# Optimization experiments

Hardware: AMD Instinct MI355X
Metric: run time of the kernel (lower is better)

## Reference

```python
import jax, jax.numpy as jnp
import numpy as np

B, S, D, H = 2, 2048, 1024, 16
DK = D // H

def setup_inputs() -> dict:
    key = jax.random.key(0)
    ks = jax.random.split(key, 11)
    scale = 1.0 / np.sqrt(D)
    inp = {
        'query': jax.random.normal(ks[0], (B, S, D), jnp.float32),
        'key':   jax.random.normal(ks[1], (B, S, D), jnp.float32),
        'value': jax.random.normal(ks[2], (B, S, D), jnp.float32),
        'wq': jax.random.normal(ks[3], (D, D), jnp.float32) * scale,
        'bq': jax.random.normal(ks[4], (D,), jnp.float32) * 0.01,
        'wk': jax.random.normal(ks[5], (D, D), jnp.float32) * scale,
        'bk': jax.random.normal(ks[6], (D,), jnp.float32) * 0.01,
        'wv': jax.random.normal(ks[7], (D, D), jnp.float32) * scale,
        'bv': jax.random.normal(ks[8], (D,), jnp.float32) * 0.01,
        'wo': jax.random.normal(ks[9], (D, D), jnp.float32) * scale,
        'bo': jax.random.normal(ks[10], (D,), jnp.float32) * 0.01,
    }
    return inp

def reference(query, key, value, wq, bq, wk, bk, wv, bv, wo, bo):
    nb = query.shape[0]
    # projections: torch nn.Linear computes x @ W^T + b; here weights stored as (in,out)
    def proj(x, w, b):
        return (x @ w + b).reshape(nb, -1, H, DK).transpose(0, 2, 1, 3)  # [B,H,S,dk]
    q = proj(query, wq, bq)
    k = proj(key, wk, bk)
    v = proj(value, wv, bv)
    scores = jnp.einsum('bhqd,bhkd->bhqk', q, k) / jnp.sqrt(jnp.float32(DK))
    p = jax.nn.softmax(scores, axis=-1)  # dropout p=0 (eval)
    x = jnp.einsum('bhqk,bhkd->bhqd', p, v)
    x = x.transpose(0, 2, 1, 3).reshape(nb, -1, H * DK)
    return x @ wo + bo
```

## Files before the change

### kernel.cpp

```cpp
#include <hip/hip_runtime.h>


typedef __attribute__((ext_vector_type(8))) __bf16 bf16x8;
typedef __attribute__((ext_vector_type(4))) __bf16 bf16x4;
typedef __attribute__((ext_vector_type(8))) float f32x8;
typedef __attribute__((ext_vector_type(4))) float f32x4;
typedef __attribute__((ext_vector_type(16))) float f32x16;
typedef unsigned uv2 __attribute__((ext_vector_type(2)));

#define MFMA16 __builtin_amdgcn_mfma_f32_16x16x32_bf16
#define MFMA32 __builtin_amdgcn_mfma_f32_32x32x16_bf16

union Bf8 { bf16x8 v; __bf16 e[8]; };

__device__ inline f32x4 zero4() { f32x4 z; z[0]=z[1]=z[2]=z[3]=0.f; return z; }
__device__ inline f32x16 zero16() {
    f32x16 z;
#pragma unroll
    for (int i = 0; i < 16; i++) z[i] = 0.f;
    return z;
}

__device__ inline float fast_exp2(float x) {
#if __has_builtin(__builtin_amdgcn_exp2f)
    return __builtin_amdgcn_exp2f(x);
#else
    return __expf(x * 0.6931471805599453f);
#endif
}

#if __has_builtin(__builtin_amdgcn_permlane32_swap)
#define HAVE_PLSWAP 1
#endif

__device__ inline void plswap32(unsigned &a, unsigned &b) {
#ifdef HAVE_PLSWAP
    uv2 r = __builtin_amdgcn_permlane32_swap(a, b, false, false);
    a = r[0]; b = r[1];
#else
    unsigned sa = __shfl_xor((int)a, 32), sb = __shfl_xor((int)b, 32);
    bool hi = (threadIdx.x & 32) != 0;
    unsigned na = hi ? sb : a;
    unsigned nb = hi ? b : sa;
    a = na; b = nb;
#endif
}

__device__ inline float red32_sum(float x) {
#ifdef HAVE_PLSWAP
    unsigned a = __float_as_uint(x), b = __float_as_uint(x);
    uv2 r = __builtin_amdgcn_permlane32_swap(a, b, false, false);
    return __uint_as_float(r[0]) + __uint_as_float(r[1]);
#else
    return x + __shfl_xor(x, 32);
#endif
}

__device__ inline unsigned pk2(float a, float b) {
    union { unsigned u; __bf16 e[2]; } r;
    r.e[0] = (__bf16)a; r.e[1] = (__bf16)b;
    return r.u;
}

__device__ inline void load_lds16(const void* g, void* l) {
    __builtin_amdgcn_global_load_lds(
        (const __attribute__((address_space(1))) unsigned int*)g,
        (__attribute__((address_space(3))) unsigned int*)l, 16, 0, 0);
}

__global__ __launch_bounds__(256) void prep_all(
        const float* __restrict__ w0, const float* __restrict__ w1,
        const float* __restrict__ w2, const float* __restrict__ w3,
        const float* __restrict__ x0, const float* __restrict__ x1,
        const float* __restrict__ x2,
        __bf16* __restrict__ wt, __bf16* __restrict__ d0,
        __bf16* __restrict__ d1, __bf16* __restrict__ d2) {
    const int z = blockIdx.z, t = threadIdx.x;
    if (z < 4) {
        const float* src = z == 0 ? w0 : z == 1 ? w1 : z == 2 ? w2 : w3;
        __bf16* dst = wt + (size_t)z * 1048576;
        __shared__ float tile[32][33];
        const int tc = t & 31, tr = t >> 5;
        const int r0 = blockIdx.y * 32, c0 = blockIdx.x * 32;
#pragma unroll
        for (int i = 0; i < 4; i++) {
            int r = tr + i * 8;
            tile[r][tc] = src[(size_t)(r0 + r) * 1024 + c0 + tc];
        }
        __syncthreads();
#pragma unroll
        for (int i = 0; i < 4; i++) {
            int r = tr + i * 8;
            dst[(size_t)(c0 + r) * 1024 + r0 + tc] = (__bf16)tile[tc][r];
        }
    } else {
        const float* src = z == 4 ? x0 : z == 5 ? x1 : x2;
        __bf16* dst = z == 4 ? d0 : z == 5 ? d1 : d2;
        int bid = blockIdx.y * 32 + blockIdx.x;
        size_t g = ((size_t)bid * 256 + t) * 16;
#pragma unroll
        for (int h = 0; h < 2; h++) {
            f32x8 a = *(const f32x8*)&src[g + h * 8];
            Bf8 tmp;
#pragma unroll
            for (int j = 0; j < 8; j++) tmp.e[j] = (__bf16)a[j];
            *(bf16x8*)&dst[g + h * 8] = tmp.v;
        }
    }
}

template <int MODE, typename OutT>
__device__ inline void gemm_fast_core(__bf16* __restrict__ smem,
                                      const __bf16* __restrict__ A,
                                      const __bf16* __restrict__ Bt,
                                      const float* __restrict__ bias,
                                      OutT* __restrict__ out, float scale) {
    __bf16* As = smem;
    __bf16* Bs = smem + 8192;
    const int t = threadIdx.x;
    const int wave = t >> 6, lane = t & 63, lm = lane & 15, quad = lane >> 4;
    const int m0 = blockIdx.y * 128, n0 = blockIdx.x * 128;
    const int wm = (wave >> 1) * 64, wn = (wave & 1) * 64;

    f32x4 acc[4][4];
#pragma unroll
    for (int i = 0; i < 4; i++)
#pragma unroll
        for (int j = 0; j < 4; j++) acc[i][j] = zero4();

    for (int k0 = 0; k0 < 1024; k0 += 64) {
#pragma unroll
        for (int i = 0; i < 4; i++) {
            int s = i * 256 + t;
            int row = s >> 3, cb = (s & 7) ^ (row & 7);
            size_t goff = (size_t)row * 1024 + k0 + cb * 8;
            load_lds16(&A[(size_t)m0 * 1024 + goff],
                       &As[(size_t)(i * 256 + wave * 64) * 8]);
            load_lds16(&Bt[(size_t)n0 * 1024 + goff],
                       &Bs[(size_t)(i * 256 + wave * 64) * 8]);
        }
        __syncthreads();
#pragma unroll
        for (int ks = 0; ks < 2; ks++) {
            bf16x8 af[4], bfr[4];
#pragma unroll
            for (int mt = 0; mt < 4; mt++)
                af[mt] = *(const bf16x8*)&As[(wm + mt * 16 + lm) * 64 +
                                             (((ks * 4 + quad) ^ (lm & 7)) * 8)];
#pragma unroll
            for (int nt = 0; nt < 4; nt++)
                bfr[nt] = *(const bf16x8*)&Bs[(wn + nt * 16 + lm) * 64 +
                                              (((ks * 4 + quad) ^ (lm & 7)) * 8)];
#pragma unroll
            for (int mt = 0; mt < 4; mt++)
#pragma unroll
                for (int nt = 0; nt < 4; nt++)
                    acc[mt][nt] = MFMA16(af[mt], bfr[nt], acc[mt][nt], 0, 0, 0);
        }
        __syncthreads();
    }

    float bv4[4];
#pragma unroll
    for (int nt = 0; nt < 4; nt++) bv4[nt] = bias[n0 + wn + nt * 16 + lm];

    if (MODE == 2) {
#pragma unroll
        for (int mt = 0; mt < 4; mt++)
#pragma unroll
            for (int r = 0; r < 4; r++) {
                int rr = wm + mt * 16 + quad * 4 + r;
#pragma unroll
                for (int nt = 0; nt < 4; nt++) {
                    int c = wn + nt * 16 + lm;
                    smem[c * 128 + (rr ^ (8 * (c & 15)))] =
                        (__bf16)((acc[mt][nt][r] + bv4[nt]) * scale);
                }
            }
        __syncthreads();
        const int b = m0 >> 11;
#pragma unroll
        for (int it = 0; it < 8; it++) {
            int g = it * 256 + t;
            int c = g >> 4, gr = g & 15;
            bf16x8 v = *(const bf16x8*)&smem[c * 128 + ((gr * 8) ^ (8 * (c & 15)))];
            int col = n0 + c, hh = col >> 6, dk = col & 63;
            int sglob = (m0 & 2047) + gr * 8;
            size_t idx = (size_t)(b * 16 + hh) * 131072 + (size_t)dk * 2048 + sglob;
            *(bf16x8*)&out[idx] = v;
        }
    } else {
#pragma unroll
        for (int mt = 0; mt < 4; mt++) {
#pragma unroll
            for (int r = 0; r < 4; r++) {
                int row = m0 + wm + mt * 16 + quad * 4 + r;
#pragma unroll
                for (int nt = 0; nt < 4; nt++) {
                    int col = n0 + wn + nt * 16 + lm;
                    float val = (acc[mt][nt][r] + bv4[nt]) * scale;
                    size_t idx;
                    if (MODE == 0) {
                        idx = (size_t)row * 1024 + col;
                    } else {
                        int b = row >> 11, s = row & 2047, hh = col >> 6, dk = col & 63;
                        idx = (size_t)(b * 16 + hh) * 131072 + (size_t)s * 64 + dk;
                    }
                    out[idx] = (OutT)val;
                }
            }
        }
    }
}

__global__ __launch_bounds__(256) void proj_fast3(
        const __bf16* __restrict__ xq, const __bf16* __restrict__ xk,
        const __bf16* __restrict__ xv, const __bf16* __restrict__ WT,
        const float* __restrict__ bq, const float* __restrict__ bk,
        const float* __restrict__ bv,
        __bf16* __restrict__ Q, __bf16* __restrict__ K, __bf16* __restrict__ Vt) {
    __shared__ __bf16 smem[16384];
    int z = blockIdx.z;
    if (z == 0)
        gemm_fast_core<1, __bf16>(smem, xq, WT, bq, Q, 0.18033688f);
    else if (z == 1)
        gemm_fast_core<1, __bf16>(smem, xk, WT + 1048576, bk, K, 1.f);
    else
        gemm_fast_core<2, __bf16>(smem, xv, WT + 2097152, bv, Vt, 1.f);
}

__global__ __launch_bounds__(256) void out_proj_fast64(
        const __bf16* __restrict__ A, const __bf16* __restrict__ Bt,
        const float* __restrict__ bias, float* __restrict__ out) {
    __shared__ __bf16 As[8192];
    __shared__ __bf16 Bs[4096];
    const int t = threadIdx.x;
    const int wave = t >> 6, lane = t & 63, lm = lane & 15, quad = lane >> 4;
    const int m0 = blockIdx.y * 128, n0 = blockIdx.x * 64;
    const int wm = (wave >> 1) * 64, wn = (wave & 1) * 32;

    f32x4 acc[4][2];
#pragma unroll
    for (int i = 0; i < 4; i++) { acc[i][0] = zero4(); acc[i][1] = zero4(); }

    for (int k0 = 0; k0 < 1024; k0 += 64) {
#pragma unroll
        for (int i = 0; i < 4; i++) {
            int s = i * 256 + t;
            int row = s >> 3, cb = (s & 7) ^ (row & 7);
            load_lds16(&A[(size_t)(m0 + row) * 1024 + k0 + cb * 8],
                       &As[(size_t)(i * 256 + wave * 64) * 8]);
            if (i < 2)
                load_lds16(&Bt[(size_t)(n0 + row) * 1024 + k0 + cb * 8],
                           &Bs[(size_t)(i * 256 + wave * 64) * 8]);
        }
        __syncthreads();
#pragma unroll
        for (int ks = 0; ks < 2; ks++) {
            bf16x8 af[4], bfr[2];
#pragma unroll
            for (int mt = 0; mt < 4; mt++)
                af[mt] = *(const bf16x8*)&As[(wm + mt * 16 + lm) * 64 +
                                             (((ks * 4 + quad) ^ (lm & 7)) * 8)];
#pragma unroll
            for (int nt = 0; nt < 2; nt++)
                bfr[nt] = *(const bf16x8*)&Bs[(wn + nt * 16 + lm) * 64 +
                                              (((ks * 4 + quad) ^ (lm & 7)) * 8)];
#pragma unroll
            for (int mt = 0; mt < 4; mt++)
#pragma unroll
                for (int nt = 0; nt < 2; nt++)
                    acc[mt][nt] = MFMA16(af[mt], bfr[nt], acc[mt][nt], 0, 0, 0);
        }
        __syncthreads();
    }

    float bv2[2];
#pragma unroll
    for (int nt = 0; nt < 2; nt++) bv2[nt] = bias[n0 + wn + nt * 16 + lm];

#pragma unroll
    for (int mt = 0; mt < 4; mt++)
#pragma unroll
        for (int r = 0; r < 4; r++) {
            int row = m0 + wm + mt * 16 + quad * 4 + r;
#pragma unroll
            for (int nt = 0; nt < 2; nt++) {
                int col = n0 + wn + nt * 16 + lm;
                out[(size_t)row * 1024 + col] = acc[mt][nt][r] + bv2[nt];
            }
        }
}

__global__ __launch_bounds__(256, 2) void attn_kernel(
        const __bf16* __restrict__ Q, const __bf16* __restrict__ K,
        const __bf16* __restrict__ Vt, __bf16* __restrict__ O) {
    __shared__ __bf16 smem[16384];
    const int t = threadIdx.x;
    const int wave = t >> 6, lane = t & 63;
    const int l31 = lane & 31, h = lane >> 5;
    const int q0 = blockIdx.x * 128;
    const int bh = blockIdx.y;
    const size_t base = (size_t)bh * 131072;

    bf16x8 bq[4];
    {
        int qrow = q0 + wave * 32 + l31;
#pragma unroll
        for (int kst = 0; kst < 4; kst++)
            bq[kst] = *(const bf16x8*)&Q[base + (size_t)qrow * 64 + kst * 16 + h * 8];
    }

    unsigned fo[4];
#pragma unroll
    for (int k = 0; k < 4; k++)
        fo[k] = (unsigned)(l31 * 64 +
                (((k * 2 + h) ^ (l31 & 7) ^ ((l31 >> 3) & 3)) * 8));

    unsigned kdst[2], ksrc[2], vsrc[2];
#pragma unroll
    for (int i = 0; i < 2; i++) {
        int s = i * 256 + t;
        int row = s >> 3, cb = (s & 7) ^ (row & 7) ^ ((row >> 3) & 3);
        kdst[i] = (unsigned)((i * 256 + wave * 64) * 8);
        ksrc[i] = (unsigned)(row * 64 + cb * 8);
        vsrc[i] = (unsigned)(row * 2048 + cb * 8);
    }

    float m_run = 0.f, l_run = 0.f;
    f32x16 o_acc[2];
    o_acc[0] = zero16();
    o_acc[1] = zero16();
    bf16x8 bp[4];

#pragma unroll
    for (int i = 0; i < 2; i++)
        load_lds16(&K[base + ksrc[i]], &smem[kdst[i]]);
    __syncthreads();

    auto body = [&](int it, int cur) {
        const int kv0 = it * 64;
        if (it < 31) {
#pragma unroll
            for (int i = 0; i < 2; i++)
                load_lds16(&K[base + (size_t)(kv0 + 64) * 64 + ksrc[i]],
                           &smem[(cur ^ 1) * 4096 + kdst[i]]);
        }
#pragma unroll
        for (int i = 0; i < 2; i++)
            load_lds16(&Vt[base + (size_t)kv0 + vsrc[i]],
                       &smem[8192 + cur * 4096 + kdst[i]]);

        f32x16 sc[2];
        sc[0] = zero16();
        sc[1] = zero16();
        __builtin_amdgcn_s_setprio(1);
#pragma unroll
        for (int mtk = 0; mtk < 2; mtk++)
#pragma unroll
            for (int kst = 0; kst < 4; kst++) {
                bf16x8 ak = *(const bf16x8*)&smem[cur * 4096 + mtk * 2048 + fo[kst]];
                sc[mtk] = MFMA32(ak, bq[kst], sc[mtk], 0, 0, 0);
            }
        if (it > 0) {
#pragma unroll
            for (int kb = 0; kb < 4; kb++)
#pragma unroll
                for (int mtd = 0; mtd < 2; mtd++) {
                    bf16x8 av = *(const bf16x8*)&smem[8192 + (cur ^ 1) * 4096 +
                                                      mtd * 2048 + fo[kb]];
                    o_acc[mtd] = MFMA32(av, bp[kb], o_acc[mtd], 0, 0, 0);
                }
        }
        __builtin_amdgcn_s_setprio(0);

#pragma unroll
        for (int mtk = 0; mtk < 2; mtk++)
#pragma unroll
            for (int r = 0; r < 16; r++)
                sc[mtk][r] = fast_exp2(sc[mtk][r] - m_run);
        float tr8[8];
#pragma unroll
        for (int i = 0; i < 8; i++)
            tr8[i] = (sc[0][i] + sc[0][i + 8]) + (sc[1][i] + sc[1][i + 8]);
#pragma unroll
        for (int st = 4; st >= 1; st >>= 1)
#pragma unroll
            for (int i = 0; i < st; i++) tr8[i] += tr8[i + st];
        float su = tr8[0];
        if (!__all(su <= 1048576.f)) {
            float pm8[8];
#pragma unroll
            for (int i = 0; i < 8; i++)
                pm8[i] = fmaxf(fmaxf(sc[0][i], sc[0][i + 8]),
                               fmaxf(sc[1][i], sc[1][i + 8]));
#pragma unroll
            for (int st = 4; st >= 1; st >>= 1)
#pragma unroll
                for (int i = 0; i < st; i++) pm8[i] = fmaxf(pm8[i], pm8[i + st]);
            float pmax = pm8[0];
#ifdef HAVE_PLSWAP
            {
                unsigned a = __float_as_uint(pmax), b = a;
                uv2 rr = __builtin_amdgcn_permlane32_swap(a, b, false, false);
                pmax = fmaxf(__uint_as_float(rr[0]), __uint_as_float(rr[1]));
            }
#else
            pmax = fmaxf(pmax, __shfl_xor(pmax, 32));
#endif
            float alpha = 1.f / pmax;
            m_run += __log2f(pmax);
#pragma unroll
            for (int mtk = 0; mtk < 2; mtk++)
#pragma unroll
                for (int r = 0; r < 16; r++) sc[mtk][r] *= alpha;
#pragma unroll
            for (int mtd = 0; mtd < 2; mtd++)
#pragma unroll
                for (int r = 0; r < 16; r++) o_acc[mtd][r] *= alpha;
            l_run *= alpha;
            su *= alpha;
        }
        l_run += su;

#pragma unroll
        for (int kb = 0; kb < 4; kb++) {
            const int mt = kb >> 1, g = (kb & 1) * 2;
            unsigned A0 = pk2(sc[mt][g * 4 + 0], sc[mt][g * 4 + 1]);
            unsigned A1 = pk2(sc[mt][g * 4 + 2], sc[mt][g * 4 + 3]);
            unsigned B0 = pk2(sc[mt][g * 4 + 4], sc[mt][g * 4 + 5]);
            unsigned B1 = pk2(sc[mt][g * 4 + 6], sc[mt][g * 4 + 7]);
            plswap32(A0, B0);
            plswap32(A1, B1);
            union { unsigned u[4]; bf16x8 v; } bb;
            bb.u[0] = A0; bb.u[1] = A1; bb.u[2] = B0; bb.u[3] = B1;
            bp[kb] = bb.v;
        }

        __syncthreads();
    };

    for (int it = 0; it < 32; it += 2) {
        body(it, 0);
        body(it + 1, 1);
    }

    {
        __builtin_amdgcn_s_setprio(1);
#pragma unroll
        for (int kb = 0; kb < 4; kb++)
#pragma unroll
            for (int mtd = 0; mtd < 2; mtd++) {
                bf16x8 av = *(const bf16x8*)&smem[8192 + 4096 + mtd * 2048 + fo[kb]];
                o_acc[mtd] = MFMA32(av, bp[kb], o_acc[mtd], 0, 0, 0);
            }
        __builtin_amdgcn_s_setprio(0);
    }
    __syncthreads();

    {
        float inv = 1.f / red32_sum(l_run);
        __bf16* Osc = &smem[wave * 2176];
#pragma unroll
        for (int mtd = 0; mtd < 2; mtd++)
#pragma unroll
            for (int c = 0; c < 4; c++) {
                bf16x4 pk4;
#pragma unroll
                for (int r2 = 0; r2 < 4; r2++)
                    pk4[r2] = (__bf16)(o_acc[mtd][c * 4 + r2] * inv);
                *(bf16x4*)&Osc[l31 * 68 + mtd * 32 + c * 8 + h * 4] = pk4;
            }
        __asm__ volatile("" ::: "memory");
        const int b = bh >> 4, hh = bh & 15;
        int ql = lane >> 1, half = lane & 1;
        int srow = q0 + wave * 32 + ql;
#pragma unroll
        for (int j = 0; j < 4; j++) {
            bf16x8 v = *(const bf16x8*)&Osc[ql * 68 + half * 32 + j * 8];
            *(bf16x8*)&O[(size_t)(b * 2048 + srow) * 1024 + hh * 64 + half * 32 + j * 8] = v;
        }
    }
}

extern "C" void kernel_launch(void* const* d_in, const int* in_sizes, int n_in,
                              void* d_out, int out_size, void* d_ws, size_t ws_size,
                              hipStream_t stream) {
    if (ws_size < ((size_t)40 << 20)) return;

    const float* query = (const float*)d_in[0];
    const float* key_  = (const float*)d_in[1];
    const float* value = (const float*)d_in[2];
    const float* wq = (const float*)d_in[3];
    const float* bq = (const float*)d_in[4];
    const float* wk = (const float*)d_in[5];
    const float* bk = (const float*)d_in[6];
    const float* wv = (const float*)d_in[7];
    const float* bv = (const float*)d_in[8];
    const float* wo = (const float*)d_in[9];
    const float* bo = (const float*)d_in[10];
    float* out = (float*)d_out;

    char* ws = (char*)d_ws;
    __bf16* WT  = (__bf16*)(ws);
    __bf16* Qw  = (__bf16*)(ws + ((size_t)8  << 20));
    __bf16* Kw  = (__bf16*)(ws + ((size_t)16 << 20));
    __bf16* Vtw = (__bf16*)(ws + ((size_t)24 << 20));
    __bf16* Ow  = (__bf16*)(ws + ((size_t)32 << 20));

    __bf16* Xq = Ow;
    __bf16* Xk = (__bf16*)d_out;
    __bf16* Xv = (__bf16*)d_out + 4194304;

    prep_all<<<dim3(32, 32, 7), dim3(256), 0, stream>>>(
        wq, wk, wv, wo, query, key_, value, WT, Xq, Xk, Xv);
    proj_fast3<<<dim3(8, 32, 3), dim3(256), 0, stream>>>(
        Xq, Xk, Xv, WT, bq, bk, bv, Qw, Kw, Vtw);
    attn_kernel<<<dim3(16, 32), dim3(256), 0, stream>>>(Qw, Kw, Vtw, Ow);
    out_proj_fast64<<<dim3(16, 32), dim3(256), 0, stream>>>(
        Ow, WT + 3 * 1048576, bo, out);
}
```

Before: 224.2 us.

## Double KV tile to 128 keys per iteration with new V swizzle

```diff
diff --git a/kernel.cpp b/kernel.cpp
--- a/kernel.cpp
+++ b/kernel.cpp
@@ -295,7 +295,7 @@
 __global__ __launch_bounds__(256, 2) void attn_kernel(
         const __bf16* __restrict__ Q, const __bf16* __restrict__ K,
         const __bf16* __restrict__ Vt, __bf16* __restrict__ O) {
-    __shared__ __bf16 smem[16384];
+    __shared__ __bf16 smem[32768];
     const int t = threadIdx.x;
     const int wave = t >> 6, lane = t & 63;
     const int l31 = lane & 31, h = lane >> 5;
@@ -317,88 +317,102 @@
         fo[k] = (unsigned)(l31 * 64 +
                 (((k * 2 + h) ^ (l31 & 7) ^ ((l31 >> 3) & 3)) * 8));
 
-    unsigned kdst[2], ksrc[2], vsrc[2];
-#pragma unroll
-    for (int i = 0; i < 2; i++) {
+    const unsigned vrow = (unsigned)(l31 * 128);
+    const unsigned hy = (unsigned)(h ^ (l31 & 15));
+
+    unsigned dst4[4], ksrc4[4], vsrc4[4];
+#pragma unroll
+    for (int i = 0; i < 4; i++) {
         int s = i * 256 + t;
-        int row = s >> 3, cb = (s & 7) ^ (row & 7) ^ ((row >> 3) & 3);
-        kdst[i] = (unsigned)((i * 256 + wave * 64) * 8);
-        ksrc[i] = (unsigned)(row * 64 + cb * 8);
-        vsrc[i] = (unsigned)(row * 2048 + cb * 8);
+        int kr = s >> 3, kcb = (s & 7) ^ (kr & 7) ^ ((kr >> 3) & 3);
+        int vr = s >> 4, vcb = (s & 15) ^ (vr & 15);
+        dst4[i] = (unsigned)((i * 256 + wave * 64) * 8);
+        ksrc4[i] = (unsigned)(kr * 64 + kcb * 8);
+        vsrc4[i] = (unsigned)(vr * 2048 + vcb * 8);
     }
 
     float m_run = 0.f, l_run = 0.f;
+    bool rescaled = false;
     f32x16 o_acc[2];
     o_acc[0] = zero16();
     o_acc[1] = zero16();
-    bf16x8 bp[4];
-
-#pragma unroll
-    for (int i = 0; i < 2; i++)
-        load_lds16(&K[base + ksrc[i]], &smem[kdst[i]]);
+    bf16x8 bp[8];
+
+    auto stageK = [&](int buf, int kv0) {
+#pragma unroll
+        for (int i = 0; i < 4; i++)
+            load_lds16(&K[base + (size_t)kv0 * 64 + ksrc4[i]],
+                       &smem[buf * 8192 + dst4[i]]);
+    };
+    auto stageV = [&](int buf, int kv0) {
+#pragma unroll
+        for (int i = 0; i < 4; i++)
+            load_lds16(&Vt[base + (size_t)kv0 + vsrc4[i]],
+                       &smem[16384 + buf * 8192 + dst4[i]]);
+    };
+
+    stageK(0, 0);
     __syncthreads();
 
     auto body = [&](int it, int cur) {
-        const int kv0 = it * 64;
-        if (it < 31) {
-#pragma unroll
-            for (int i = 0; i < 2; i++)
-                load_lds16(&K[base + (size_t)(kv0 + 64) * 64 + ksrc[i]],
-                           &smem[(cur ^ 1) * 4096 + kdst[i]]);
-        }
-#pragma unroll
-        for (int i = 0; i < 2; i++)
-            load_lds16(&Vt[base + (size_t)kv0 + vsrc[i]],
-                       &smem[8192 + cur * 4096 + kdst[i]]);
-
-        f32x16 sc[2];
-        sc[0] = zero16();
-        sc[1] = zero16();
+        const int kv0 = it * 128;
+        if (it < 15) stageK(cur ^ 1, kv0 + 128);
+        stageV(cur, kv0);
+
+        f32x16 sc[4];
+#pragma unroll
+        for (int m = 0; m < 4; m++) sc[m] = zero16();
         __builtin_amdgcn_s_setprio(1);
 #pragma unroll
-        for (int mtk = 0; mtk < 2; mtk++)
+        for (int mtk = 0; mtk < 4; mtk++)
 #pragma unroll
             for (int kst = 0; kst < 4; kst++) {
-                bf16x8 ak = *(const bf16x8*)&smem[cur * 4096 + mtk * 2048 + fo[kst]];
+                bf16x8 ak = *(const bf16x8*)&smem[cur * 8192 + mtk * 2048 + fo[kst]];
                 sc[mtk] = MFMA32(ak, bq[kst], sc[mtk], 0, 0, 0);
             }
         if (it > 0) {
 #pragma unroll
-            for (int kb = 0; kb < 4; kb++)
+            for (int kb = 0; kb < 8; kb++)
 #pragma unroll
                 for (int mtd = 0; mtd < 2; mtd++) {
-                    bf16x8 av = *(const bf16x8*)&smem[8192 + (cur ^ 1) * 4096 +
-                                                      mtd * 2048 + fo[kb]];
+                    bf16x8 av = *(const bf16x8*)&smem[16384 + (cur ^ 1) * 8192 +
+                                                      mtd * 4096 + vrow +
+                                                      (((kb * 2) ^ hy) * 8)];
                     o_acc[mtd] = MFMA32(av, bp[kb], o_acc[mtd], 0, 0, 0);
                 }
         }
         __builtin_amdgcn_s_setprio(0);
 
-#pragma unroll
-        for (int mtk = 0; mtk < 2; mtk++)
-#pragma unroll
-            for (int r = 0; r < 16; r++)
-                sc[mtk][r] = fast_exp2(sc[mtk][r] - m_run);
-        float tr8[8];
-#pragma unroll
-        for (int i = 0; i < 8; i++)
-            tr8[i] = (sc[0][i] + sc[0][i + 8]) + (sc[1][i] + sc[1][i + 8]);
-#pragma unroll
-        for (int st = 4; st >= 1; st >>= 1)
-#pragma unroll
-            for (int i = 0; i < st; i++) tr8[i] += tr8[i + st];
-        float su = tr8[0];
+        if (!rescaled) {
+#pragma unroll
+            for (int m = 0; m < 4; m++)
+#pragma unroll
+                for (int r = 0; r < 16; r++) sc[m][r] = fast_exp2(sc[m][r]);
+        } else {
+#pragma unroll
+            for (int m = 0; m < 4; m++)
+#pragma unroll
+                for (int r = 0; r < 16; r++) sc[m][r] = fast_exp2(sc[m][r] - m_run);
+        }
+        float tr[16];
+#pragma unroll
+        for (int i = 0; i < 16; i++)
+            tr[i] = (sc[0][i] + sc[1][i]) + (sc[2][i] + sc[3][i]);
+#pragma unroll
+        for (int st = 8; st >= 1; st >>= 1)
+#pragma unroll
+            for (int i = 0; i < st; i++) tr[i] += tr[i + st];
+        float su = tr[0];
         if (!__all(su <= 1048576.f)) {
-            float pm8[8];
-#pragma unroll
-            for (int i = 0; i < 8; i++)
-                pm8[i] = fmaxf(fmaxf(sc[0][i], sc[0][i + 8]),
-                               fmaxf(sc[1][i], sc[1][i + 8]));
-#pragma unroll
-            for (int st = 4; st >= 1; st >>= 1)
-#pragma unroll
-                for (int i = 0; i < st; i++) pm8[i] = fmaxf(pm8[i], pm8[i + st]);
-            float pmax = pm8[0];
+            float pm[16];
+#pragma unroll
+            for (int i = 0; i < 16; i++)
+                pm[i] = fmaxf(fmaxf(sc[0][i], sc[1][i]), fmaxf(sc[2][i], sc[3][i]));
+#pragma unroll
+            for (int st = 8; st >= 1; st >>= 1)
+#pragma unroll
+                for (int i = 0; i < st; i++) pm[i] = fmaxf(pm[i], pm[i + st]);
+            float pmax = pm[0];
 #ifdef HAVE_PLSWAP
             {
                 unsigned a = __float_as_uint(pmax), b = a;
@@ -410,10 +424,11 @@
 #endif
             float alpha = 1.f / pmax;
             m_run += __log2f(pmax);
-#pragma unroll
-            for (int mtk = 0; mtk < 2; mtk++)
-#pragma unroll
-                for (int r = 0; r < 16; r++) sc[mtk][r] *= alpha;
+            rescaled = true;
+#pragma unroll
+            for (int m = 0; m < 4; m++)
+#pragma unroll
+                for (int r = 0; r < 16; r++) sc[m][r] *= alpha;
 #pragma unroll
             for (int mtd = 0; mtd < 2; mtd++)
 #pragma unroll
@@ -424,7 +439,7 @@
         l_run += su;
 
 #pragma unroll
-        for (int kb = 0; kb < 4; kb++) {
+        for (int kb = 0; kb < 8; kb++) {
             const int mt = kb >> 1, g = (kb & 1) * 2;
             unsigned A0 = pk2(sc[mt][g * 4 + 0], sc[mt][g * 4 + 1]);
             unsigned A1 = pk2(sc[mt][g * 4 + 2], sc[mt][g * 4 + 3]);
@@ -440,7 +455,7 @@
         __syncthreads();
     };
 
-    for (int it = 0; it < 32; it += 2) {
+    for (int it = 0; it < 16; it += 2) {
         body(it, 0);
         body(it + 1, 1);
     }
@@ -448,10 +463,11 @@
     {
         __builtin_amdgcn_s_setprio(1);
 #pragma unroll
-        for (int kb = 0; kb < 4; kb++)
+        for (int kb = 0; kb < 8; kb++)
 #pragma unroll
             for (int mtd = 0; mtd < 2; mtd++) {
-                bf16x8 av = *(const bf16x8*)&smem[8192 + 4096 + mtd * 2048 + fo[kb]];
+                bf16x8 av = *(const bf16x8*)&smem[16384 + 8192 + mtd * 4096 + vrow +
+                                                  (((kb * 2) ^ hy) * 8)];
                 o_acc[mtd] = MFMA32(av, bp[kb], o_acc[mtd], 0, 0, 0);
             }
         __builtin_amdgcn_s_setprio(0);
```

After: 224.6 us. No clear change (+0.2%).
